# Kernel optimization log

Hardware: AMD Instinct MI355X
Metric: run time of the kernel (lower is better)

## Reference

```python
import jax, jax.numpy as jnp
import numpy as np

N_NODES = 100000
N_EDGES = 1600000
DIM = 64
LAYERS = 2


def setup_inputs() -> dict:
    key = jax.random.key(0)
    k1, k2, k3, k4 = jax.random.split(key, 4)
    h = jax.random.normal(k1, (N_NODES, DIM), dtype=jnp.float32)
    w = jax.random.uniform(k2, (N_EDGES,), dtype=jnp.float32)
    src = jax.random.randint(k3, (N_EDGES,), 0, N_NODES, dtype=jnp.int32)
    dst = jax.random.randint(k4, (N_EDGES,), 0, N_NODES, dtype=jnp.int32)
    return {"h": h, "w": w, "src": src, "dst": dst}


def reference(h, w, src, dst):
    N = h.shape[0]
    # weighted in-degree, clamped at 1 (DGL in_degrees(weight='w').clamp(min=1))
    deg = jnp.maximum(jax.ops.segment_sum(w, dst, num_segments=N), 1.0)
    norm = deg[:, None] ** -0.5  # [N, 1]
    embs = [h]
    for _ in range(LAYERS):
        h_norm = h * norm                              # [N, d]
        m = h_norm[src] * w[:, None]                   # [E, d] edge messages (u_mul_e)
        neigh_sum = jax.ops.segment_sum(m, dst, num_segments=N)  # fn.sum
        h = neigh_sum * norm
        embs.append(h)
    # mean over [h0, h1, ..., hL]
    return jnp.mean(jnp.stack(embs, axis=1), axis=1)
```

## Files before the change

kernel.cpp:

```cpp
#include <hip/hip_runtime.h>
#include <hip/hip_bf16.h>

#define D 64
#define THREADS 256
#define BKT_BITS 9
#define BKT_NODES (1 << BKT_BITS)
#define CHUNK 8192

__device__ __forceinline__ unsigned f2bf(float f) {
    unsigned u = __float_as_uint(f);
    return (u + 0x7fffu + ((u >> 16) & 1u)) >> 16;
}
__device__ __forceinline__ float2 bfpair(unsigned v) {
    return make_float2(__uint_as_float(v << 16), __uint_as_float(v & 0xffff0000u));
}

__global__ void p1a_hist(const int* __restrict__ dst, int* __restrict__ blockCount,
                         int E, int B) {
    __shared__ int lc[256];
    int t = threadIdx.x;
    lc[t] = 0;
    __syncthreads();
    int base = blockIdx.x * CHUNK;
    int end = min(base + CHUNK, E);
    for (int e = base + t; e < end; e += THREADS)
        atomicAdd(&lc[dst[e] >> BKT_BITS], 1);
    __syncthreads();
    if (t < B) blockCount[(long long)blockIdx.x * B + t] = lc[t];
}

__global__ void p1b_scanblocks(int* __restrict__ blockCount, int* __restrict__ total,
                               int NBLK, int B) {
    __shared__ int sm[256];
    int b = blockIdx.x, t = threadIdx.x;
    int run = 0;
    for (int base = 0; base < NBLK; base += 256) {
        int i = base + t;
        int v = (i < NBLK) ? blockCount[(long long)i * B + b] : 0;
        sm[t] = v;
        __syncthreads();
        for (int off = 1; off < 256; off <<= 1) {
            int u = (t >= off) ? sm[t - off] : 0;
            __syncthreads();
            sm[t] += u;
            __syncthreads();
        }
        if (i < NBLK) blockCount[(long long)i * B + b] = run + sm[t] - v;
        run += sm[255];
        __syncthreads();
    }
    if (t == 0) total[b] = run;
}

__global__ void p1c_scanbuckets(const int* __restrict__ total, int* __restrict__ bstart,
                                int B, int E) {
    __shared__ int sm[256];
    int t = threadIdx.x;
    int run = 0;
    for (int base = 0; base < B; base += 256) {
        int i = base + t;
        int v = (i < B) ? total[i] : 0;
        sm[t] = v;
        __syncthreads();
        for (int off = 1; off < 256; off <<= 1) {
            int u = (t >= off) ? sm[t - off] : 0;
            __syncthreads();
            sm[t] += u;
            __syncthreads();
        }
        if (i < B) bstart[i] = run + sm[t] - v;
        run += sm[255];
        __syncthreads();
    }
    if (t == 0) bstart[B] = E;
}

__global__ void p1d_scatter(const int* __restrict__ dst, const int* __restrict__ src,
                            const float* __restrict__ w, const int* __restrict__ blockCount,
                            const int* __restrict__ bstart, int2* __restrict__ temp,
                            int E, int B) {
    __shared__ int cur[256];
    int t = threadIdx.x;
    if (t < B) cur[t] = bstart[t] + blockCount[(long long)blockIdx.x * B + t];
    __syncthreads();
    int base = blockIdx.x * CHUNK;
    int end = min(base + CHUNK, E);
    for (int e = base + t; e < end; e += THREADS) {
        int d = dst[e];
        int b = d >> BKT_BITS;
        int pos = atomicAdd(&cur[b], 1);
        temp[pos] = make_int2(src[e] | ((d & (BKT_NODES - 1)) << 17),
                              __float_as_int(w[e]));
    }
}

__global__ void p2_build(const int2* __restrict__ temp, const int* __restrict__ bstart,
                         int2* __restrict__ packed, int* __restrict__ rowptr,
                         float* __restrict__ norm, int N, int E, int B) {
    __shared__ int cnt[BKT_NODES];
    __shared__ float degs[BKT_NODES];
    __shared__ int cur[BKT_NODES];
    __shared__ int sm[256];
    int b = blockIdx.x, t = threadIdx.x;
    int ebeg = bstart[b], eend = bstart[b + 1];
    for (int i = t; i < BKT_NODES; i += THREADS) { cnt[i] = 0; degs[i] = 0.0f; }
    __syncthreads();
    for (int e = ebeg + t; e < eend; e += THREADS) {
        int2 pk = temp[e];
        int dl = (pk.x >> 17) & (BKT_NODES - 1);
        atomicAdd(&cnt[dl], 1);
        atomicAdd(&degs[dl], __int_as_float(pk.y));
    }
    __syncthreads();
    int run = 0;
    for (int base = 0; base < BKT_NODES; base += 256) {
        int v = cnt[base + t];
        sm[t] = v;
        __syncthreads();
        for (int off = 1; off < 256; off <<= 1) {
            int u = (t >= off) ? sm[t - off] : 0;
            __syncthreads();
            sm[t] += u;
            __syncthreads();
        }
        cur[base + t] = run + sm[t] - v;
        run += sm[255];
        __syncthreads();
    }
    int node0 = b << BKT_BITS;
    for (int i = t; i < BKT_NODES; i += THREADS) {
        int node = node0 + i;
        if (node < N) {
            rowptr[node] = ebeg + cur[i];
            norm[node] = rsqrtf(fmaxf(degs[i], 1.0f));
        }
    }
    if (b == 0 && t == 0) rowptr[N] = E;
    __syncthreads();
    for (int e = ebeg + t; e < eend; e += THREADS) {
        int2 pk = temp[e];
        int dl = (pk.x >> 17) & (BKT_NODES - 1);
        int pos = atomicAdd(&cur[dl], 1);
        packed[ebeg + pos] = make_int2(pk.x & 0x1ffff, pk.y);
    }
}

__global__ void tobf16_kernel(const float* __restrict__ h, unsigned* __restrict__ hbf2,
                              long long nd4) {
    long long i = (long long)blockIdx.x * blockDim.x + threadIdx.x;
    if (i < nd4) {
        float4 v = ((const float4*)h)[i];
        ((uint2*)hbf2)[i] = make_uint2(f2bf(v.x) | (f2bf(v.y) << 16),
                                       f2bf(v.z) | (f2bf(v.w) << 16));
    }
}

__global__ void gather1_kernel(const uint2* __restrict__ h_in, const int2* __restrict__ packed,
                               const int* __restrict__ rowptr, const float* __restrict__ norm,
                               uint2* __restrict__ h_out, int N) {
    int node = blockIdx.x * (blockDim.x >> 4) + (threadIdx.x >> 4);
    int lane = threadIdx.x & 15;
    if (node >= N) return;
    int j = rowptr[node], end = rowptr[node + 1];
    float a00 = 0, a01 = 0, a02 = 0, a03 = 0;
    float a10 = 0, a11 = 0, a12 = 0, a13 = 0;
    float a20 = 0, a21 = 0, a22 = 0, a23 = 0;
    float a30 = 0, a31 = 0, a32 = 0, a33 = 0;
    for (; j + 4 <= end; j += 4) {
        int2 p0 = packed[j], p1 = packed[j + 1], p2 = packed[j + 2], p3 = packed[j + 3];
        uint2 r0 = h_in[((long long)p0.x << 4) + lane];
        uint2 r1 = h_in[((long long)p1.x << 4) + lane];
        uint2 r2 = h_in[((long long)p2.x << 4) + lane];
        uint2 r3 = h_in[((long long)p3.x << 4) + lane];
        float c0 = __int_as_float(p0.y) * norm[p0.x];
        float c1 = __int_as_float(p1.y) * norm[p1.x];
        float c2 = __int_as_float(p2.y) * norm[p2.x];
        float c3 = __int_as_float(p3.y) * norm[p3.x];
        float2 f0a = bfpair(r0.x), f0b = bfpair(r0.y);
        float2 f1a = bfpair(r1.x), f1b = bfpair(r1.y);
        float2 f2a = bfpair(r2.x), f2b = bfpair(r2.y);
        float2 f3a = bfpair(r3.x), f3b = bfpair(r3.y);
        a00 = fmaf(f0a.x, c0, a00); a01 = fmaf(f0a.y, c0, a01);
        a02 = fmaf(f0b.x, c0, a02); a03 = fmaf(f0b.y, c0, a03);
        a10 = fmaf(f1a.x, c1, a10); a11 = fmaf(f1a.y, c1, a11);
        a12 = fmaf(f1b.x, c1, a12); a13 = fmaf(f1b.y, c1, a13);
        a20 = fmaf(f2a.x, c2, a20); a21 = fmaf(f2a.y, c2, a21);
        a22 = fmaf(f2b.x, c2, a22); a23 = fmaf(f2b.y, c2, a23);
        a30 = fmaf(f3a.x, c3, a30); a31 = fmaf(f3a.y, c3, a31);
        a32 = fmaf(f3b.x, c3, a32); a33 = fmaf(f3b.y, c3, a33);
    }
    for (; j < end; ++j) {
        int2 p = packed[j];
        uint2 r = h_in[((long long)p.x << 4) + lane];
        float c = __int_as_float(p.y) * norm[p.x];
        float2 fa = bfpair(r.x), fb = bfpair(r.y);
        a00 = fmaf(fa.x, c, a00); a01 = fmaf(fa.y, c, a01);
        a02 = fmaf(fb.x, c, a02); a03 = fmaf(fb.y, c, a03);
    }
    float nv = norm[node];
    float d0 = ((a00 + a10) + (a20 + a30)) * nv;
    float d1 = ((a01 + a11) + (a21 + a31)) * nv;
    float d2 = ((a02 + a12) + (a22 + a32)) * nv;
    float d3 = ((a03 + a13) + (a23 + a33)) * nv;
    h_out[((long long)node << 4) + lane] =
        make_uint2(f2bf(d0) | (f2bf(d1) << 16), f2bf(d2) | (f2bf(d3) << 16));
}

__global__ void gather2_final_kernel(const uint2* __restrict__ h0bf, const uint2* __restrict__ h1bf,
                                     const int2* __restrict__ packed, const int* __restrict__ rowptr,
                                     const float* __restrict__ norm, float* __restrict__ out, int N) {
    int node = blockIdx.x * (blockDim.x >> 4) + (threadIdx.x >> 4);
    int lane = threadIdx.x & 15;
    if (node >= N) return;
    int j = rowptr[node], end = rowptr[node + 1];
    float a00 = 0, a01 = 0, a02 = 0, a03 = 0;
    float a10 = 0, a11 = 0, a12 = 0, a13 = 0;
    float a20 = 0, a21 = 0, a22 = 0, a23 = 0;
    float a30 = 0, a31 = 0, a32 = 0, a33 = 0;
    for (; j + 4 <= end; j += 4) {
        int2 p0 = packed[j], p1 = packed[j + 1], p2 = packed[j + 2], p3 = packed[j + 3];
        uint2 r0 = h1bf[((long long)p0.x << 4) + lane];
        uint2 r1 = h1bf[((long long)p1.x << 4) + lane];
        uint2 r2 = h1bf[((long long)p2.x << 4) + lane];
        uint2 r3 = h1bf[((long long)p3.x << 4) + lane];
        float c0 = __int_as_float(p0.y) * norm[p0.x];
        float c1 = __int_as_float(p1.y) * norm[p1.x];
        float c2 = __int_as_float(p2.y) * norm[p2.x];
        float c3 = __int_as_float(p3.y) * norm[p3.x];
        float2 f0a = bfpair(r0.x), f0b = bfpair(r0.y);
        float2 f1a = bfpair(r1.x), f1b = bfpair(r1.y);
        float2 f2a = bfpair(r2.x), f2b = bfpair(r2.y);
        float2 f3a = bfpair(r3.x), f3b = bfpair(r3.y);
        a00 = fmaf(f0a.x, c0, a00); a01 = fmaf(f0a.y, c0, a01);
        a02 = fmaf(f0b.x, c0, a02); a03 = fmaf(f0b.y, c0, a03);
        a10 = fmaf(f1a.x, c1, a10); a11 = fmaf(f1a.y, c1, a11);
        a12 = fmaf(f1b.x, c1, a12); a13 = fmaf(f1b.y, c1, a13);
        a20 = fmaf(f2a.x, c2, a20); a21 = fmaf(f2a.y, c2, a21);
        a22 = fmaf(f2b.x, c2, a22); a23 = fmaf(f2b.y, c2, a23);
        a30 = fmaf(f3a.x, c3, a30); a31 = fmaf(f3a.y, c3, a31);
        a32 = fmaf(f3b.x, c3, a32); a33 = fmaf(f3b.y, c3, a33);
    }
    for (; j < end; ++j) {
        int2 p = packed[j];
        uint2 r = h1bf[((long long)p.x << 4) + lane];
        float c = __int_as_float(p.y) * norm[p.x];
        float2 fa = bfpair(r.x), fb = bfpair(r.y);
        a00 = fmaf(fa.x, c, a00); a01 = fmaf(fa.y, c, a01);
        a02 = fmaf(fb.x, c, a02); a03 = fmaf(fb.y, c, a03);
    }
    long long idx = ((long long)node << 4) + lane;
    float nv = norm[node];
    uint2 h0r = h0bf[idx], h1r = h1bf[idx];
    float2 h0a = bfpair(h0r.x), h0b = bfpair(h0r.y);
    float2 h1a = bfpair(h1r.x), h1b = bfpair(h1r.y);
    float4 o;
    o.x = (h0a.x + h1a.x + ((a00 + a10) + (a20 + a30)) * nv) * (1.0f / 3.0f);
    o.y = (h0a.y + h1a.y + ((a01 + a11) + (a21 + a31)) * nv) * (1.0f / 3.0f);
    o.z = (h0b.x + h1b.x + ((a02 + a12) + (a22 + a32)) * nv) * (1.0f / 3.0f);
    o.w = (h0b.y + h1b.y + ((a03 + a13) + (a23 + a33)) * nv) * (1.0f / 3.0f);
    ((float4*)out)[idx] = o;
}

extern "C" void kernel_launch(void* const* d_in, const int* in_sizes, int n_in,
                              void* d_out, int out_size, void* d_ws, size_t ws_size,
                              hipStream_t stream) {
    const float* h   = (const float*)d_in[0];
    const float* w   = (const float*)d_in[1];
    const int*   src = (const int*)d_in[2];
    const int*   dst = (const int*)d_in[3];
    const int N = in_sizes[0] / D;
    const int E = in_sizes[1];
    float* out = (float*)d_out;

    const int B = (N + BKT_NODES - 1) >> BKT_BITS;
    const int NBLK = (E + CHUNK - 1) / CHUNK;

    char* ws = (char*)d_ws;
    size_t off = 0;
    auto alloc = [&](size_t bytes, size_t align) -> char* {
        off = (off + align - 1) & ~(align - 1);
        char* p = ws + off;
        off += bytes;
        return p;
    };
    float* norm     = (float*)alloc((size_t)N * 4, 16);
    int*   rowptr   = (int*)  alloc((size_t)(N + 1) * 4, 16);
    int*   total    = (int*)  alloc((size_t)B * 4, 16);
    int*   bstart   = (int*)  alloc((size_t)(B + 1) * 4, 16);
    int*   blockCnt = (int*)  alloc((size_t)NBLK * B * 4, 16);
    int2*  packed   = (int2*) alloc((size_t)E * 8, 16);
    char*  shared_region = alloc((size_t)E * 8, 128);
    int2*     temp = (int2*)shared_region;
    unsigned* h1bf = (unsigned*)shared_region;
    unsigned* h0bf = (unsigned*)alloc((size_t)N * D * 2, 128);

    const int nodes_per_block = THREADS / 16;
    const int gather_blocks = (N + nodes_per_block - 1) / nodes_per_block;
    const long long nd4 = (long long)N * D / 4;
    const int cvt_blocks = (int)((nd4 + THREADS - 1) / THREADS);

    p1a_hist<<<NBLK, THREADS, 0, stream>>>(dst, blockCnt, E, B);
    p1b_scanblocks<<<B, 256, 0, stream>>>(blockCnt, total, NBLK, B);
    p1c_scanbuckets<<<1, 256, 0, stream>>>(total, bstart, B, E);
    p1d_scatter<<<NBLK, THREADS, 0, stream>>>(dst, src, w, blockCnt, bstart, temp, E, B);
    p2_build<<<B, 256, 0, stream>>>(temp, bstart, packed, rowptr, norm, N, E, B);

    tobf16_kernel<<<cvt_blocks, THREADS, 0, stream>>>(h, h0bf, nd4);

    gather1_kernel<<<gather_blocks, THREADS, 0, stream>>>((const uint2*)h0bf, packed, rowptr,
                                                          norm, (uint2*)h1bf, N);
    gather2_final_kernel<<<gather_blocks, THREADS, 0, stream>>>((const uint2*)h0bf, (const uint2*)h1bf,
                                                                packed, rowptr, norm, out, N);
}
```

Before: 238.3 us.

## Precompute per-edge source-norm coefficients and widen gathers to 16-byte loads

Splits the CSR build into two kernels so every node's norm exists before edge placement. The placement kernel then stores w*norm[src] directly in the packed edge array, which removes the per-edge norm lookup from both gather kernels. The gathers switch from 16 lanes of 8-byte loads to 8 lanes of 16-byte loads per node and unroll over 8 edges. This trades an extra kernel launch and a random norm read during placement for fewer, wider irregular loads in the hot gathers.

```diff
diff --git a/kernel.cpp b/kernel.cpp
--- a/kernel.cpp
+++ b/kernel.cpp
@@ -94,12 +94,11 @@
     }
 }
 
-__global__ void p2_build(const int2* __restrict__ temp, const int* __restrict__ bstart,
-                         int2* __restrict__ packed, int* __restrict__ rowptr,
-                         float* __restrict__ norm, int N, int E, int B) {
+__global__ void p2a_build(const int2* __restrict__ temp, const int* __restrict__ bstart,
+                          int* __restrict__ rowptr, float* __restrict__ norm,
+                          int N, int E, int B) {
     __shared__ int cnt[BKT_NODES];
     __shared__ float degs[BKT_NODES];
-    __shared__ int cur[BKT_NODES];
     __shared__ int sm[256];
     int b = blockIdx.x, t = threadIdx.x;
     int ebeg = bstart[b], eend = bstart[b + 1];
@@ -112,6 +111,7 @@
         atomicAdd(&degs[dl], __int_as_float(pk.y));
     }
     __syncthreads();
+    int node0 = b << BKT_BITS;
     int run = 0;
     for (int base = 0; base < BKT_NODES; base += 256) {
         int v = cnt[base + t];
@@ -123,25 +123,36 @@
             sm[t] += u;
             __syncthreads();
         }
-        cur[base + t] = run + sm[t] - v;
+        int node = node0 + base + t;
+        if (node < N) {
+            rowptr[node] = ebeg + run + sm[t] - v;
+            norm[node] = rsqrtf(fmaxf(degs[base + t], 1.0f));
+        }
         run += sm[255];
         __syncthreads();
     }
+    if (b == 0 && t == 0) rowptr[N] = E;
+}
+
+__global__ void p2b_place(const int2* __restrict__ temp, const int* __restrict__ bstart,
+                          const int* __restrict__ rowptr, const float* __restrict__ norm,
+                          int2* __restrict__ packed, int N, int E) {
+    __shared__ int cur[BKT_NODES];
+    int b = blockIdx.x, t = threadIdx.x;
+    int ebeg = bstart[b], eend = bstart[b + 1];
     int node0 = b << BKT_BITS;
     for (int i = t; i < BKT_NODES; i += THREADS) {
         int node = node0 + i;
-        if (node < N) {
-            rowptr[node] = ebeg + cur[i];
-            norm[node] = rsqrtf(fmaxf(degs[i], 1.0f));
-        }
-    }
-    if (b == 0 && t == 0) rowptr[N] = E;
+        cur[i] = (node < N) ? (rowptr[node] - ebeg) : 0;
+    }
     __syncthreads();
     for (int e = ebeg + t; e < eend; e += THREADS) {
         int2 pk = temp[e];
         int dl = (pk.x >> 17) & (BKT_NODES - 1);
+        int s = pk.x & 0x1ffff;
+        float coef = __int_as_float(pk.y) * norm[s];
         int pos = atomicAdd(&cur[dl], 1);
-        packed[ebeg + pos] = make_int2(pk.x & 0x1ffff, pk.y);
+        packed[ebeg + pos] = make_int2(s, __float_as_int(coef));
     }
 }
 
@@ -155,110 +166,128 @@
     }
 }
 
-__global__ void gather1_kernel(const uint2* __restrict__ h_in, const int2* __restrict__ packed,
+#define EDGE_FMA(r, c, A0, A1, A2, A3, A4, A5, A6, A7) do {            \
+    float2 fa = bfpair((r).x), fb = bfpair((r).y);                      \
+    float2 fc = bfpair((r).z), fd = bfpair((r).w);                      \
+    A0 = fmaf(fa.x, (c), A0); A1 = fmaf(fa.y, (c), A1);                 \
+    A2 = fmaf(fb.x, (c), A2); A3 = fmaf(fb.y, (c), A3);                 \
+    A4 = fmaf(fc.x, (c), A4); A5 = fmaf(fc.y, (c), A5);                 \
+    A6 = fmaf(fd.x, (c), A6); A7 = fmaf(fd.y, (c), A7); } while (0)
+
+__global__ void gather1_kernel(const uint4* __restrict__ h_in, const int2* __restrict__ packed,
                                const int* __restrict__ rowptr, const float* __restrict__ norm,
-                               uint2* __restrict__ h_out, int N) {
-    int node = blockIdx.x * (blockDim.x >> 4) + (threadIdx.x >> 4);
-    int lane = threadIdx.x & 15;
+                               uint4* __restrict__ h_out, int N) {
+    int node = blockIdx.x * (blockDim.x >> 3) + (threadIdx.x >> 3);
+    int lane = threadIdx.x & 7;
     if (node >= N) return;
     int j = rowptr[node], end = rowptr[node + 1];
-    float a00 = 0, a01 = 0, a02 = 0, a03 = 0;
-    float a10 = 0, a11 = 0, a12 = 0, a13 = 0;
-    float a20 = 0, a21 = 0, a22 = 0, a23 = 0;
-    float a30 = 0, a31 = 0, a32 = 0, a33 = 0;
+    float a0 = 0, a1 = 0, a2 = 0, a3 = 0, a4 = 0, a5 = 0, a6 = 0, a7 = 0;
+    float b0 = 0, b1 = 0, b2 = 0, b3 = 0, b4 = 0, b5 = 0, b6 = 0, b7 = 0;
+    for (; j + 8 <= end; j += 8) {
+        int2 p0 = packed[j + 0], p1 = packed[j + 1], p2 = packed[j + 2], p3 = packed[j + 3];
+        int2 p4 = packed[j + 4], p5 = packed[j + 5], p6 = packed[j + 6], p7 = packed[j + 7];
+        uint4 r0 = h_in[((long long)p0.x << 3) + lane];
+        uint4 r1 = h_in[((long long)p1.x << 3) + lane];
+        uint4 r2 = h_in[((long long)p2.x << 3) + lane];
+        uint4 r3 = h_in[((long long)p3.x << 3) + lane];
+        uint4 r4 = h_in[((long long)p4.x << 3) + lane];
+        uint4 r5 = h_in[((long long)p5.x << 3) + lane];
+        uint4 r6 = h_in[((long long)p6.x << 3) + lane];
+        uint4 r7 = h_in[((long long)p7.x << 3) + lane];
+        EDGE_FMA(r0, __int_as_float(p0.y), a0, a1, a2, a3, a4, a5, a6, a7);
+        EDGE_FMA(r1, __int_as_float(p1.y), b0, b1, b2, b3, b4, b5, b6, b7);
+        EDGE_FMA(r2, __int_as_float(p2.y), a0, a1, a2, a3, a4, a5, a6, a7);
+        EDGE_FMA(r3, __int_as_float(p3.y), b0, b1, b2, b3, b4, b5, b6, b7);
+        EDGE_FMA(r4, __int_as_float(p4.y), a0, a1, a2, a3, a4, a5, a6, a7);
+        EDGE_FMA(r5, __int_as_float(p5.y), b0, b1, b2, b3, b4, b5, b6, b7);
+        EDGE_FMA(r6, __int_as_float(p6.y), a0, a1, a2, a3, a4, a5, a6, a7);
+        EDGE_FMA(r7, __int_as_float(p7.y), b0, b1, b2, b3, b4, b5, b6, b7);
+    }
     for (; j + 4 <= end; j += 4) {
-        int2 p0 = packed[j], p1 = packed[j + 1], p2 = packed[j + 2], p3 = packed[j + 3];
-        uint2 r0 = h_in[((long long)p0.x << 4) + lane];
-        uint2 r1 = h_in[((long long)p1.x << 4) + lane];
-        uint2 r2 = h_in[((long long)p2.x << 4) + lane];
-        uint2 r3 = h_in[((long long)p3.x << 4) + lane];
-        float c0 = __int_as_float(p0.y) * norm[p0.x];
-        float c1 = __int_as_float(p1.y) * norm[p1.x];
-        float c2 = __int_as_float(p2.y) * norm[p2.x];
-        float c3 = __int_as_float(p3.y) * norm[p3.x];
-        float2 f0a = bfpair(r0.x), f0b = bfpair(r0.y);
-        float2 f1a = bfpair(r1.x), f1b = bfpair(r1.y);
-        float2 f2a = bfpair(r2.x), f2b = bfpair(r2.y);
-        float2 f3a = bfpair(r3.x), f3b = bfpair(r3.y);
-        a00 = fmaf(f0a.x, c0, a00); a01 = fmaf(f0a.y, c0, a01);
-        a02 = fmaf(f0b.x, c0, a02); a03 = fmaf(f0b.y, c0, a03);
-        a10 = fmaf(f1a.x, c1, a10); a11 = fmaf(f1a.y, c1, a11);
-        a12 = fmaf(f1b.x, c1, a12); a13 = fmaf(f1b.y, c1, a13);
-        a20 = fmaf(f2a.x, c2, a20); a21 = fmaf(f2a.y, c2, a21);
-        a22 = fmaf(f2b.x, c2, a22); a23 = fmaf(f2b.y, c2, a23);
-        a30 = fmaf(f3a.x, c3, a30); a31 = fmaf(f3a.y, c3, a31);
-        a32 = fmaf(f3b.x, c3, a32); a33 = fmaf(f3b.y, c3, a33);
+        int2 p0 = packed[j + 0], p1 = packed[j + 1], p2 = packed[j + 2], p3 = packed[j + 3];
+        uint4 r0 = h_in[((long long)p0.x << 3) + lane];
+        uint4 r1 = h_in[((long long)p1.x << 3) + lane];
+        uint4 r2 = h_in[((long long)p2.x << 3) + lane];
+        uint4 r3 = h_in[((long long)p3.x << 3) + lane];
+        EDGE_FMA(r0, __int_as_float(p0.y), a0, a1, a2, a3, a4, a5, a6, a7);
+        EDGE_FMA(r1, __int_as_float(p1.y), b0, b1, b2, b3, b4, b5, b6, b7);
+        EDGE_FMA(r2, __int_as_float(p2.y), a0, a1, a2, a3, a4, a5, a6, a7);
+        EDGE_FMA(r3, __int_as_float(p3.y), b0, b1, b2, b3, b4, b5, b6, b7);
     }
     for (; j < end; ++j) {
         int2 p = packed[j];
-        uint2 r = h_in[((long long)p.x << 4) + lane];
-        float c = __int_as_float(p.y) * norm[p.x];
-        float2 fa = bfpair(r.x), fb = bfpair(r.y);
-        a00 = fmaf(fa.x, c, a00); a01 = fmaf(fa.y, c, a01);
-        a02 = fmaf(fb.x, c, a02); a03 = fmaf(fb.y, c, a03);
+        uint4 r = h_in[((long long)p.x << 3) + lane];
+        EDGE_FMA(r, __int_as_float(p.y), a0, a1, a2, a3, a4, a5, a6, a7);
     }
     float nv = norm[node];
-    float d0 = ((a00 + a10) + (a20 + a30)) * nv;
-    float d1 = ((a01 + a11) + (a21 + a31)) * nv;
-    float d2 = ((a02 + a12) + (a22 + a32)) * nv;
-    float d3 = ((a03 + a13) + (a23 + a33)) * nv;
-    h_out[((long long)node << 4) + lane] =
-        make_uint2(f2bf(d0) | (f2bf(d1) << 16), f2bf(d2) | (f2bf(d3) << 16));
-}
-
-__global__ void gather2_final_kernel(const uint2* __restrict__ h0bf, const uint2* __restrict__ h1bf,
+    float d0 = (a0 + b0) * nv, d1 = (a1 + b1) * nv, d2 = (a2 + b2) * nv, d3 = (a3 + b3) * nv;
+    float d4 = (a4 + b4) * nv, d5 = (a5 + b5) * nv, d6 = (a6 + b6) * nv, d7 = (a7 + b7) * nv;
+    h_out[((long long)node << 3) + lane] =
+        make_uint4(f2bf(d0) | (f2bf(d1) << 16), f2bf(d2) | (f2bf(d3) << 16),
+                   f2bf(d4) | (f2bf(d5) << 16), f2bf(d6) | (f2bf(d7) << 16));
+}
+
+__global__ void gather2_final_kernel(const uint4* __restrict__ h0bf, const uint4* __restrict__ h1bf,
                                      const int2* __restrict__ packed, const int* __restrict__ rowptr,
                                      const float* __restrict__ norm, float* __restrict__ out, int N) {
-    int node = blockIdx.x * (blockDim.x >> 4) + (threadIdx.x >> 4);
-    int lane = threadIdx.x & 15;
+    int node = blockIdx.x * (blockDim.x >> 3) + (threadIdx.x >> 3);
+    int lane = threadIdx.x & 7;
     if (node >= N) return;
     int j = rowptr[node], end = rowptr[node + 1];
-    float a00 = 0, a01 = 0, a02 = 0, a03 = 0;
-    float a10 = 0, a11 = 0, a12 = 0, a13 = 0;
-    float a20 = 0, a21 = 0, a22 = 0, a23 = 0;
-    float a30 = 0, a31 = 0, a32 = 0, a33 = 0;
+    float a0 = 0, a1 = 0, a2 = 0, a3 = 0, a4 = 0, a5 = 0, a6 = 0, a7 = 0;
+    float b0 = 0, b1 = 0, b2 = 0, b3 = 0, b4 = 0, b5 = 0, b6 = 0, b7 = 0;
+    for (; j + 8 <= end; j += 8) {
+        int2 p0 = packed[j + 0], p1 = packed[j + 1], p2 = packed[j + 2], p3 = packed[j + 3];
+        int2 p4 = packed[j + 4], p5 = packed[j + 5], p6 = packed[j + 6], p7 = packed[j + 7];
+        uint4 r0 = h1bf[((long long)p0.x << 3) + lane];
+        uint4 r1 = h1bf[((long long)p1.x << 3) + lane];
+        uint4 r2 = h1bf[((long long)p2.x << 3) + lane];
+        uint4 r3 = h1bf[((long long)p3.x << 3) + lane];
+        uint4 r4 = h1bf[((long long)p4.x << 3) + lane];
+        uint4 r5 = h1bf[((long long)p5.x << 3) + lane];
+        uint4 r6 = h1bf[((long long)p6.x << 3) + lane];
+        uint4 r7 = h1bf[((long long)p7.x << 3) + lane];
+        EDGE_FMA(r0, __int_as_float(p0.y), a0, a1, a2, a3, a4, a5, a6, a7);
+        EDGE_FMA(r1, __int_as_float(p1.y), b0, b1, b2, b3, b4, b5, b6, b7);
+        EDGE_FMA(r2, __int_as_float(p2.y), a0, a1, a2, a3, a4, a5, a6, a7);
+        EDGE_FMA(r3, __int_as_float(p3.y), b0, b1, b2, b3, b4, b5, b6, b7);
+        EDGE_FMA(r4, __int_as_float(p4.y), a0, a1, a2, a3, a4, a5, a6, a7);
+        EDGE_FMA(r5, __int_as_float(p5.y), b0, b1, b2, b3, b4, b5, b6, b7);
+        EDGE_FMA(r6, __int_as_float(p6.y), a0, a1, a2, a3, a4, a5, a6, a7);
+        EDGE_FMA(r7, __int_as_float(p7.y), b0, b1, b2, b3, b4, b5, b6, b7);
+    }
     for (; j + 4 <= end; j += 4) {
-        int2 p0 = packed[j], p1 = packed[j + 1], p2 = packed[j + 2], p3 = packed[j + 3];
-        uint2 r0 = h1bf[((long long)p0.x << 4) + lane];
-        uint2 r1 = h1bf[((long long)p1.x << 4) + lane];
-        uint2 r2 = h1bf[((long long)p2.x << 4) + lane];
-        uint2 r3 = h1bf[((long long)p3.x << 4) + lane];
-        float c0 = __int_as_float(p0.y) * norm[p0.x];
-        float c1 = __int_as_float(p1.y) * norm[p1.x];
-        float c2 = __int_as_float(p2.y) * norm[p2.x];
-        float c3 = __int_as_float(p3.y) * norm[p3.x];
-        float2 f0a = bfpair(r0.x), f0b = bfpair(r0.y);
-        float2 f1a = bfpair(r1.x), f1b = bfpair(r1.y);
-        float2 f2a = bfpair(r2.x), f2b = bfpair(r2.y);
-        float2 f3a = bfpair(r3.x), f3b = bfpair(r3.y);
-        a00 = fmaf(f0a.x, c0, a00); a01 = fmaf(f0a.y, c0, a01);
-        a02 = fmaf(f0b.x, c0, a02); a03 = fmaf(f0b.y, c0, a03);
-        a10 = fmaf(f1a.x, c1, a10); a11 = fmaf(f1a.y, c1, a11);
-        a12 = fmaf(f1b.x, c1, a12); a13 = fmaf(f1b.y, c1, a13);
-        a20 = fmaf(f2a.x, c2, a20); a21 = fmaf(f2a.y, c2, a21);
-        a22 = fmaf(f2b.x, c2, a22); a23 = fmaf(f2b.y, c2, a23);
-        a30 = fmaf(f3a.x, c3, a30); a31 = fmaf(f3a.y, c3, a31);
-        a32 = fmaf(f3b.x, c3, a32); a33 = fmaf(f3b.y, c3, a33);
+        int2 p0 = packed[j + 0], p1 = packed[j + 1], p2 = packed[j + 2], p3 = packed[j + 3];
+        uint4 r0 = h1bf[((long long)p0.x << 3) + lane];
+        uint4 r1 = h1bf[((long long)p1.x << 3) + lane];
+        uint4 r2 = h1bf[((long long)p2.x << 3) + lane];
+        uint4 r3 = h1bf[((long long)p3.x << 3) + lane];
+        EDGE_FMA(r0, __int_as_float(p0.y), a0, a1, a2, a3, a4, a5, a6, a7);
+        EDGE_FMA(r1, __int_as_float(p1.y), b0, b1, b2, b3, b4, b5, b6, b7);
+        EDGE_FMA(r2, __int_as_float(p2.y), a0, a1, a2, a3, a4, a5, a6, a7);
+        EDGE_FMA(r3, __int_as_float(p3.y), b0, b1, b2, b3, b4, b5, b6, b7);
     }
     for (; j < end; ++j) {
         int2 p = packed[j];
-        uint2 r = h1bf[((long long)p.x << 4) + lane];
-        float c = __int_as_float(p.y) * norm[p.x];
-        float2 fa = bfpair(r.x), fb = bfpair(r.y);
-        a00 = fmaf(fa.x, c, a00); a01 = fmaf(fa.y, c, a01);
-        a02 = fmaf(fb.x, c, a02); a03 = fmaf(fb.y, c, a03);
-    }
-    long long idx = ((long long)node << 4) + lane;
+        uint4 r = h1bf[((long long)p.x << 3) + lane];
+        EDGE_FMA(r, __int_as_float(p.y), a0, a1, a2, a3, a4, a5, a6, a7);
+    }
+    long long idx = ((long long)node << 3) + lane;
     float nv = norm[node];
-    uint2 h0r = h0bf[idx], h1r = h1bf[idx];
-    float2 h0a = bfpair(h0r.x), h0b = bfpair(h0r.y);
-    float2 h1a = bfpair(h1r.x), h1b = bfpair(h1r.y);
-    float4 o;
-    o.x = (h0a.x + h1a.x + ((a00 + a10) + (a20 + a30)) * nv) * (1.0f / 3.0f);
-    o.y = (h0a.y + h1a.y + ((a01 + a11) + (a21 + a31)) * nv) * (1.0f / 3.0f);
-    o.z = (h0b.x + h1b.x + ((a02 + a12) + (a22 + a32)) * nv) * (1.0f / 3.0f);
-    o.w = (h0b.y + h1b.y + ((a03 + a13) + (a23 + a33)) * nv) * (1.0f / 3.0f);
-    ((float4*)out)[idx] = o;
+    uint4 h0r = h0bf[idx], h1r = h1bf[idx];
+    float2 h0a = bfpair(h0r.x), h0b = bfpair(h0r.y), h0c = bfpair(h0r.z), h0d = bfpair(h0r.w);
+    float2 h1a = bfpair(h1r.x), h1b = bfpair(h1r.y), h1c = bfpair(h1r.z), h1d = bfpair(h1r.w);
+    float4 o0, o1;
+    o0.x = (h0a.x + h1a.x + (a0 + b0) * nv) * (1.0f / 3.0f);
+    o0.y = (h0a.y + h1a.y + (a1 + b1) * nv) * (1.0f / 3.0f);
+    o0.z = (h0b.x + h1b.x + (a2 + b2) * nv) * (1.0f / 3.0f);
+    o0.w = (h0b.y + h1b.y + (a3 + b3) * nv) * (1.0f / 3.0f);
+    o1.x = (h0c.x + h1c.x + (a4 + b4) * nv) * (1.0f / 3.0f);
+    o1.y = (h0c.y + h1c.y + (a5 + b5) * nv) * (1.0f / 3.0f);
+    o1.z = (h0d.x + h1d.x + (a6 + b6) * nv) * (1.0f / 3.0f);
+    o1.w = (h0d.y + h1d.y + (a7 + b7) * nv) * (1.0f / 3.0f);
+    ((float4*)out)[((long long)node << 4) + (lane << 1)] = o0;
+    ((float4*)out)[((long long)node << 4) + (lane << 1) + 1] = o1;
 }
 
 extern "C" void kernel_launch(void* const* d_in, const int* in_sizes, int n_in,
@@ -294,7 +323,7 @@
     unsigned* h1bf = (unsigned*)shared_region;
     unsigned* h0bf = (unsigned*)alloc((size_t)N * D * 2, 128);
 
-    const int nodes_per_block = THREADS / 16;
+    const int nodes_per_block = THREADS / 8;
     const int gather_blocks = (N + nodes_per_block - 1) / nodes_per_block;
     const long long nd4 = (long long)N * D / 4;
     const int cvt_blocks = (int)((nd4 + THREADS - 1) / THREADS);
@@ -303,12 +332,13 @@
     p1b_scanblocks<<<B, 256, 0, stream>>>(blockCnt, total, NBLK, B);
     p1c_scanbuckets<<<1, 256, 0, stream>>>(total, bstart, B, E);
     p1d_scatter<<<NBLK, THREADS, 0, stream>>>(dst, src, w, blockCnt, bstart, temp, E, B);
-    p2_build<<<B, 256, 0, stream>>>(temp, bstart, packed, rowptr, norm, N, E, B);
+    p2a_build<<<B, 256, 0, stream>>>(temp, bstart, rowptr, norm, N, E, B);
+    p2b_place<<<B, 256, 0, stream>>>(temp, bstart, rowptr, norm, packed, N, E);
 
     tobf16_kernel<<<cvt_blocks, THREADS, 0, stream>>>(h, h0bf, nd4);
 
-    gather1_kernel<<<gather_blocks, THREADS, 0, stream>>>((const uint2*)h0bf, packed, rowptr,
-                                                          norm, (uint2*)h1bf, N);
-    gather2_final_kernel<<<gather_blocks, THREADS, 0, stream>>>((const uint2*)h0bf, (const uint2*)h1bf,
+    gather1_kernel<<<gather_blocks, THREADS, 0, stream>>>((const uint4*)h0bf, packed, rowptr,
+                                                          norm, (uint4*)h1bf, N);
+    gather2_final_kernel<<<gather_blocks, THREADS, 0, stream>>>((const uint4*)h0bf, (const uint4*)h1bf,
                                                                 packed, rowptr, norm, out, N);
 }
```

After: 230.7 us. 1.03x faster.
